# Kernel tuning notes

Measured on AMD Instinct MI355X. Metric: run time of the kernel, lower is better.

The kernel has to match this reference:

```python
import jax, jax.numpy as jnp
import numpy as np

EPS = 1e-6

def _conv1x1(x, w, b):
    # x: [b,c,h,w], w: [o,c], b: [o] -> per-pixel matmul
    return jnp.einsum('bchw,oc->bohw', x, w) + b[None, :, None, None]

def setup_inputs() -> dict:
    key = jax.random.key(0)
    ks = jax.random.split(key, 10)
    b, c, h, w = 16, 256, 128, 128
    dec = jax.random.normal(ks[0], (b, c, h, w), jnp.float32)
    enc = jax.random.normal(ks[1], (b, c, h, w), jnp.float32)
    ln_w = jnp.ones((c,), jnp.float32)
    ln_b = jnp.zeros((c,), jnp.float32)
    w0 = jax.random.normal(ks[2], (c, c), jnp.float32) * 0.05
    b0 = jax.random.normal(ks[3], (c,), jnp.float32) * 0.05
    w1 = jax.random.normal(ks[4], (c // 2, c), jnp.float32) * 0.05
    b1 = jax.random.normal(ks[5], (c // 2,), jnp.float32) * 0.05
    w2 = jax.random.normal(ks[6], (c // 4, c // 2), jnp.float32) * 0.05
    b2 = jax.random.normal(ks[7], (c // 4,), jnp.float32) * 0.05
    w3 = jax.random.normal(ks[8], (1, c // 4), jnp.float32) * 0.05
    b3 = jax.random.normal(ks[9], (1,), jnp.float32) * 0.05
    return dict(dec=dec, enc=enc, ln_w=ln_w, ln_b=ln_b, w0=w0, b0=b0,
                w1=w1, b1=b1, w2=w2, b2=b2, w3=w3, b3=b3)

def reference(dec, enc, ln_w, ln_b, w0, b0, w1, b1, w2, b2, w3, b3):
    b, c, h, w = dec.shape
    x = dec + enc
    # LayerNorm2d: normalize over channel dim per pixel (biased var, eps=1e-6)
    mu = jnp.mean(x, axis=1, keepdims=True)
    var = jnp.var(x, axis=1, keepdims=True)
    x = (x - mu) / jnp.sqrt(var + EPS) * ln_w[None, :, None, None] + ln_b[None, :, None, None]
    # in_conv: 1x1 conv + exact GELU
    x = jax.nn.gelu(_conv1x1(x, w0, b0), approximate=False)
    # split: local channels kept, global channels pooled and broadcast back
    local_x = x[:, :c // 2]                                   # [b,c/2,h,w]
    global_x = jnp.mean(x[:, c // 2:], axis=(2, 3), keepdims=True)  # [b,c/2,1,1]
    x = jnp.concatenate([local_x, jnp.broadcast_to(global_x, local_x.shape)], axis=1)
    # mask_pre: nc -> nc/2 -> nc/4 -> 1 with GELUs
    x = jax.nn.gelu(_conv1x1(x, w1, b1), approximate=False)
    x = jax.nn.gelu(_conv1x1(x, w2, b2), approximate=False)
    x = _conv1x1(x, w3, b3)
    return jax.nn.sigmoid(x)
```

## Files before the change

kernel.cpp:

```cpp
#include <hip/hip_runtime.h>
#include <math.h>

typedef float f32x4 __attribute__((ext_vector_type(4)));
typedef short s8v __attribute__((ext_vector_type(8)));

#define LN_EPS 1e-6f

static __device__ __forceinline__ unsigned short f2bf(float f) {
  union { float f; unsigned int u; } v; v.f = f;
  unsigned int r = (v.u + 0x7FFFu + ((v.u >> 16) & 1u)) >> 16;
  return (unsigned short)r;
}
static __device__ __forceinline__ float bf2f(unsigned short b) {
  union { float f; unsigned int u; } v; v.u = ((unsigned int)b) << 16;
  return v.f;
}
static __device__ __forceinline__ float gelu_exact(float x) {
  return 0.5f * x * (1.0f + erff(x * 0.70710678118654752f));
}

__global__ void prep_kernel(const float* __restrict__ w0, const float* __restrict__ w1,
                            const float* __restrict__ w2,
                            unsigned short* __restrict__ wt0f, unsigned short* __restrict__ w1f,
                            unsigned short* __restrict__ w2f, float* __restrict__ gacc) {
  int idx = blockIdx.x * blockDim.x + threadIdx.x;
  int stride = gridDim.x * blockDim.x;
  const int N0 = 65536, N1 = 16384, N2 = 8192, N3 = 2048;
  for (int i = idx; i < N0 + N1 + N2 + N3; i += stride) {
    if (i < N0) {
      int j = i & 7, l = (i >> 3) & 63, ks = (i >> 9) & 7, n0 = i >> 12;
      wt0f[i] = f2bf(w0[(n0 * 16 + (l & 15)) * 256 + ks * 32 + (l >> 4) * 8 + j]);
    } else if (i < N0 + N1) {
      int t = i - N0;
      int j = t & 7, l = (t >> 3) & 63, ks = (t >> 9) & 3, n0 = t >> 11;
      w1f[t] = f2bf(w1[(n0 * 16 + (l & 15)) * 256 + ks * 32 + (l >> 4) * 8 + j]);
    } else if (i < N0 + N1 + N2) {
      int t = i - N0 - N1;
      int j = t & 7, l = (t >> 3) & 63, ks = (t >> 9) & 3, n0 = t >> 11;
      w2f[t] = f2bf(w2[(n0 * 16 + (l & 15)) * 128 + ks * 32 + (l >> 4) * 8 + j]);
    } else {
      gacc[i - N0 - N1 - N2] = 0.0f;
    }
  }
}

__global__ __launch_bounds__(256, 2) void k1_kernel(
    const float* __restrict__ dec, const float* __restrict__ enc,
    const float* __restrict__ lnw, const float* __restrict__ lnb,
    const float* __restrict__ b0, const unsigned short* __restrict__ wt0f,
    unsigned short* __restrict__ yl, float* __restrict__ gacc) {
  __shared__ __align__(16) unsigned char At[64 * 512];
  __shared__ float red[16][16][8];
  __shared__ float muL[64], rsL[64];
  __shared__ float lnwS[256], lnbS[256];

  const int tid = threadIdx.x;
  const int blk = blockIdx.x;
  const int b = blk >> 8;
  const int hw0 = (blk & 255) << 6;
  const int g = tid >> 4, kq = tid & 15;
  const int lane = tid & 63, w = tid >> 6;
  const int l15 = lane & 15, lg = lane >> 4;

  lnwS[tid] = lnw[tid];
  lnbS[tid] = lnb[tid];

  f32x4 xv[16];
  f32x4 sum = {0.f, 0.f, 0.f, 0.f}, sq = {0.f, 0.f, 0.f, 0.f};
  const int baseoff = (b * 256) * 16384 + hw0 + (kq << 2);
#pragma unroll
  for (int it = 0; it < 2; ++it) {
#pragma unroll
    for (int s = 0; s < 8; ++s) {
      int c = it * 128 + g * 8 + s;
      f32x4 d = *(const f32x4*)(dec + baseoff + c * 16384);
      f32x4 e = *(const f32x4*)(enc + baseoff + c * 16384);
      f32x4 x = d + e;
      xv[it * 8 + s] = x;
      sum += x;
      sq += x * x;
    }
  }
#pragma unroll
  for (int q = 0; q < 4; ++q) { red[g][kq][q] = sum[q]; red[g][kq][4 + q] = sq[q]; }
  __syncthreads();
  if (tid < 64) {
    int p = tid, kk = p >> 2, comp = p & 3;
    float s = 0.f, s2 = 0.f;
#pragma unroll
    for (int gg = 0; gg < 16; ++gg) { s += red[gg][kk][comp]; s2 += red[gg][kk][4 + comp]; }
    float mu = s * (1.0f / 256.0f);
    float var = s2 * (1.0f / 256.0f) - mu * mu;
    muL[p] = mu;
    rsL[p] = rsqrtf(var + LN_EPS);
  }
  __syncthreads();

#pragma unroll
  for (int it = 0; it < 2; ++it) {
    int c0 = it * 128 + g * 8;
#pragma unroll
    for (int px = 0; px < 4; ++px) {
      int p = (kq << 2) + px;
      float mu = muL[p], rs = rsL[p];
      s8v hv;
#pragma unroll
      for (int s = 0; s < 8; ++s) {
        float x = xv[it * 8 + s][px];
        hv[s] = (short)f2bf((x - mu) * rs * lnwS[c0 + s] + lnbS[c0 + s]);
      }
      int byte = (p * 512 + c0 * 2) ^ ((p & 7) << 4);
      *(s8v*)(&At[byte]) = hv;
    }
  }
  __syncthreads();

  f32x4 acc[4][4];
#pragma unroll
  for (int mi = 0; mi < 4; ++mi)
#pragma unroll
    for (int ni = 0; ni < 4; ++ni) acc[mi][ni] = (f32x4){0.f, 0.f, 0.f, 0.f};

#pragma unroll
  for (int ks = 0; ks < 8; ++ks) {
    s8v a[4];
#pragma unroll
    for (int mi = 0; mi < 4; ++mi) {
      int p = mi * 16 + l15;
      int byte = (p * 512 + ks * 64 + lg * 16) ^ ((p & 7) << 4);
      a[mi] = *(const s8v*)(&At[byte]);
    }
#pragma unroll
    for (int ni = 0; ni < 4; ++ni) {
      int n0 = w * 4 + ni;
      s8v bfr = *(const s8v*)(wt0f + ((n0 * 8 + ks) * 64 + lane) * 8);
#pragma unroll
      for (int mi = 0; mi < 4; ++mi)
        acc[mi][ni] = __builtin_amdgcn_mfma_f32_16x16x32_bf16(a[mi], bfr, acc[mi][ni], 0, 0, 0);
    }
  }

  float bias[4];
#pragma unroll
  for (int ni = 0; ni < 4; ++ni) bias[ni] = b0[w * 64 + ni * 16 + l15];

  if (w < 2) {
#pragma unroll
    for (int mi = 0; mi < 4; ++mi) {
#pragma unroll
      for (int r = 0; r < 4; ++r) {
        int p = mi * 16 + lg * 4 + r;
        int prow = (b * 16384 + hw0 + p) * 128;
#pragma unroll
        for (int ni = 0; ni < 4; ++ni) {
          float v = gelu_exact(acc[mi][ni][r] + bias[ni]);
          yl[prow + w * 64 + ni * 16 + l15] = f2bf(v);
        }
      }
    }
  } else {
#pragma unroll
    for (int ni = 0; ni < 4; ++ni) {
      float ps = 0.f;
#pragma unroll
      for (int mi = 0; mi < 4; ++mi)
#pragma unroll
        for (int r = 0; r < 4; ++r)
          ps += gelu_exact(acc[mi][ni][r] + bias[ni]);
      ps += __shfl_xor(ps, 16, 64);
      ps += __shfl_xor(ps, 32, 64);
      if (lane < 16) atomicAdd(&gacc[b * 128 + (w - 2) * 64 + ni * 16 + lane], ps);
    }
  }
}

__global__ void kmid_kernel(const float* __restrict__ w1, const float* __restrict__ b1,
                            const float* __restrict__ gacc, float* __restrict__ g1) {
  int b = blockIdx.x, o = threadIdx.x;
  float acc = b1[o];
  const float inv = 1.0f / 16384.0f;
  for (int c = 0; c < 128; ++c)
    acc += w1[o * 256 + 128 + c] * (gacc[b * 128 + c] * inv);
  g1[b * 128 + o] = acc;
}

__global__ __launch_bounds__(256, 4) void k2_kernel(
    const unsigned short* __restrict__ yl, const float* __restrict__ g1,
    const float* __restrict__ b2v, const float* __restrict__ w3,
    const float* __restrict__ b3, const unsigned short* __restrict__ w1f,
    const unsigned short* __restrict__ w2f, float* __restrict__ out) {
  __shared__ __align__(16) unsigned char Yt[64 * 256];
  __shared__ __align__(16) unsigned char Z1[64 * 256];
  __shared__ __align__(16) unsigned char Z2[64 * 128];
  __shared__ float part3[4][64];
  __shared__ float w3S[64];

  const int tid = threadIdx.x, blk = blockIdx.x;
  const int lane = tid & 63, w = tid >> 6, l15 = lane & 15, lg = lane >> 4;
  const int P0 = blk * 64;
  const int b = blk >> 8;

  if (tid < 64) w3S[tid] = w3[tid];

#pragma unroll
  for (int q = 0; q < 4; ++q) {
    int p = q * 16 + (tid >> 4);
    int c2 = (tid & 15) * 16;
    s8v v = *(const s8v*)((const char*)yl + (long)(P0 + p) * 256 + c2);
    int byte = (p * 256 + c2) ^ ((p & 7) << 4);
    *(s8v*)(&Yt[byte]) = v;
  }
  __syncthreads();

  f32x4 acc1[4][2];
#pragma unroll
  for (int mi = 0; mi < 4; ++mi)
#pragma unroll
    for (int ni = 0; ni < 2; ++ni) acc1[mi][ni] = (f32x4){0.f, 0.f, 0.f, 0.f};
#pragma unroll
  for (int ks = 0; ks < 4; ++ks) {
    s8v a[4];
#pragma unroll
    for (int mi = 0; mi < 4; ++mi) {
      int p = mi * 16 + l15;
      int byte = (p * 256 + ks * 64 + lg * 16) ^ ((p & 7) << 4);
      a[mi] = *(const s8v*)(&Yt[byte]);
    }
#pragma unroll
    for (int ni = 0; ni < 2; ++ni) {
      int n0 = w * 2 + ni;
      s8v bfr = *(const s8v*)(w1f + ((n0 * 4 + ks) * 64 + lane) * 8);
#pragma unroll
      for (int mi = 0; mi < 4; ++mi)
        acc1[mi][ni] = __builtin_amdgcn_mfma_f32_16x16x32_bf16(a[mi], bfr, acc1[mi][ni], 0, 0, 0);
    }
  }
#pragma unroll
  for (int ni = 0; ni < 2; ++ni) {
    int o = (w * 2 + ni) * 16 + l15;
    float bias = g1[b * 128 + o];
#pragma unroll
    for (int mi = 0; mi < 4; ++mi)
#pragma unroll
      for (int r = 0; r < 4; ++r) {
        int p = mi * 16 + lg * 4 + r;
        float v = gelu_exact(acc1[mi][ni][r] + bias);
        int byte = (p * 256 + o * 2) ^ ((p & 7) << 4);
        *(unsigned short*)(&Z1[byte]) = f2bf(v);
      }
  }
  __syncthreads();

  f32x4 acc2[4];
#pragma unroll
  for (int mi = 0; mi < 4; ++mi) acc2[mi] = (f32x4){0.f, 0.f, 0.f, 0.f};
#pragma unroll
  for (int ks = 0; ks < 4; ++ks) {
    s8v a[4];
#pragma unroll
    for (int mi = 0; mi < 4; ++mi) {
      int p = mi * 16 + l15;
      int byte = (p * 256 + ks * 64 + lg * 16) ^ ((p & 7) << 4);
      a[mi] = *(const s8v*)(&Z1[byte]);
    }
    s8v bfr = *(const s8v*)(w2f + ((w * 4 + ks) * 64 + lane) * 8);
#pragma unroll
    for (int mi = 0; mi < 4; ++mi)
      acc2[mi] = __builtin_amdgcn_mfma_f32_16x16x32_bf16(a[mi], bfr, acc2[mi], 0, 0, 0);
  }
  {
    int o = w * 16 + l15;
    float bias = b2v[o];
#pragma unroll
    for (int mi = 0; mi < 4; ++mi)
#pragma unroll
      for (int r = 0; r < 4; ++r) {
        int p = mi * 16 + lg * 4 + r;
        float v = gelu_exact(acc2[mi][r] + bias);
        int byte = (p * 128 + o * 2) ^ ((p & 7) << 4);
        *(unsigned short*)(&Z2[byte]) = f2bf(v);
      }
  }
  __syncthreads();

  {
    int p = tid & 63, cg = tid >> 6;
    float dot = 0.f;
#pragma unroll
    for (int half = 0; half < 2; ++half) {
      int byte = (p * 128 + cg * 32 + half * 16) ^ ((p & 7) << 4);
      s8v z = *(const s8v*)(&Z2[byte]);
#pragma unroll
      for (int j = 0; j < 8; ++j)
        dot += bf2f((unsigned short)z[j]) * w3S[cg * 16 + half * 8 + j];
    }
    part3[cg][p] = dot;
  }
  __syncthreads();
  if (tid < 64) {
    float t = part3[0][tid] + part3[1][tid] + part3[2][tid] + part3[3][tid] + b3[0];
    out[P0 + tid] = 1.0f / (1.0f + expf(-t));
  }
}

extern "C" void kernel_launch(void* const* d_in, const int* in_sizes, int n_in,
                              void* d_out, int out_size, void* d_ws, size_t ws_size,
                              hipStream_t stream) {
  const float* dec = (const float*)d_in[0];
  const float* enc = (const float*)d_in[1];
  const float* lnw = (const float*)d_in[2];
  const float* lnb = (const float*)d_in[3];
  const float* w0  = (const float*)d_in[4];
  const float* b0  = (const float*)d_in[5];
  const float* w1  = (const float*)d_in[6];
  const float* b1  = (const float*)d_in[7];
  const float* w2  = (const float*)d_in[8];
  const float* b2  = (const float*)d_in[9];
  const float* w3  = (const float*)d_in[10];
  const float* b3  = (const float*)d_in[11];

  char* ws = (char*)d_ws;
  unsigned short* yl   = (unsigned short*)ws;
  unsigned short* wt0f = (unsigned short*)(ws + 67108864);
  unsigned short* w1f  = (unsigned short*)(ws + 67239936);
  unsigned short* w2f  = (unsigned short*)(ws + 67272704);
  float* gacc          = (float*)(ws + 67289088);
  float* g1            = (float*)(ws + 67297280);

  prep_kernel<<<128, 256, 0, stream>>>(w0, w1, w2, wt0f, w1f, w2f, gacc);
  k1_kernel<<<4096, 256, 0, stream>>>(dec, enc, lnw, lnb, b0, wt0f, yl, gacc);
  kmid_kernel<<<16, 128, 0, stream>>>(w1, b1, gacc, g1);
  k2_kernel<<<4096, 256, 0, stream>>>(yl, g1, b2, w3, b3, w1f, w2f, (float*)d_out);
}
```

Measured before the change: 229.4 us.

## Fold LayerNorm affine into conv weights and halve k1 pixel tile

Folds the LayerNorm scale into the first conv weights in the prep kernel, plus per-output sums for the shift and bias. The GEMM therefore runs on raw (dec+enc) cast to bf16, and normalization is applied afterwards as acc*rs + (-mu*rs)*s + t. k1 now handles 32 pixels per block instead of 64, uses wave shuffles instead of a large LDS reduction, removes a barrier before the LDS store, and raises the occupancy target to 6 blocks. The risk is precision: quantizing unnormalized x to bf16 and subtracting the mean after the GEMM can cancel badly when the mean is large relative to the spread. Halving the tile also doubles weight-fragment reloads per pixel.

```diff
diff --git a/kernel.cpp b/kernel.cpp
--- a/kernel.cpp
+++ b/kernel.cpp
@@ -20,16 +20,19 @@
 }
 
 __global__ void prep_kernel(const float* __restrict__ w0, const float* __restrict__ w1,
-                            const float* __restrict__ w2,
+                            const float* __restrict__ w2, const float* __restrict__ lnw,
+                            const float* __restrict__ lnb, const float* __restrict__ b0,
                             unsigned short* __restrict__ wt0f, unsigned short* __restrict__ w1f,
-                            unsigned short* __restrict__ w2f, float* __restrict__ gacc) {
+                            unsigned short* __restrict__ w2f, float* __restrict__ gacc,
+                            float* __restrict__ sfold, float* __restrict__ tfold) {
   int idx = blockIdx.x * blockDim.x + threadIdx.x;
   int stride = gridDim.x * blockDim.x;
-  const int N0 = 65536, N1 = 16384, N2 = 8192, N3 = 2048;
-  for (int i = idx; i < N0 + N1 + N2 + N3; i += stride) {
+  const int N0 = 65536, N1 = 16384, N2 = 8192, N3 = 2048, N4 = 256;
+  for (int i = idx; i < N0 + N1 + N2 + N3 + N4; i += stride) {
     if (i < N0) {
       int j = i & 7, l = (i >> 3) & 63, ks = (i >> 9) & 7, n0 = i >> 12;
-      wt0f[i] = f2bf(w0[(n0 * 16 + (l & 15)) * 256 + ks * 32 + (l >> 4) * 8 + j]);
+      int k = ks * 32 + (l >> 4) * 8 + j;
+      wt0f[i] = f2bf(w0[(n0 * 16 + (l & 15)) * 256 + k] * lnw[k]);
     } else if (i < N0 + N1) {
       int t = i - N0;
       int j = t & 7, l = (t >> 3) & 63, ks = (t >> 9) & 3, n0 = t >> 11;
@@ -38,138 +41,158 @@
       int t = i - N0 - N1;
       int j = t & 7, l = (t >> 3) & 63, ks = (t >> 9) & 3, n0 = t >> 11;
       w2f[t] = f2bf(w2[(n0 * 16 + (l & 15)) * 128 + ks * 32 + (l >> 4) * 8 + j]);
+    } else if (i < N0 + N1 + N2 + N3) {
+      gacc[i - N0 - N1 - N2] = 0.0f;
     } else {
-      gacc[i - N0 - N1 - N2] = 0.0f;
-    }
-  }
-}
-
-__global__ __launch_bounds__(256, 2) void k1_kernel(
+      int n = i - N0 - N1 - N2 - N3;
+      float s = 0.f, t = 0.f;
+      for (int c = 0; c < 256; ++c) {
+        float wv = w0[n * 256 + c];
+        s += wv * lnw[c];
+        t += wv * lnb[c];
+      }
+      sfold[n] = s;
+      tfold[n] = t + b0[n];
+    }
+  }
+}
+
+__global__ __launch_bounds__(256, 6) void k1_kernel(
     const float* __restrict__ dec, const float* __restrict__ enc,
-    const float* __restrict__ lnw, const float* __restrict__ lnb,
-    const float* __restrict__ b0, const unsigned short* __restrict__ wt0f,
+    const unsigned short* __restrict__ wt0f,
+    const float* __restrict__ sfold, const float* __restrict__ tfold,
     unsigned short* __restrict__ yl, float* __restrict__ gacc) {
-  __shared__ __align__(16) unsigned char At[64 * 512];
-  __shared__ float red[16][16][8];
-  __shared__ float muL[64], rsL[64];
-  __shared__ float lnwS[256], lnbS[256];
-
-  const int tid = threadIdx.x;
-  const int blk = blockIdx.x;
-  const int b = blk >> 8;
-  const int hw0 = (blk & 255) << 6;
-  const int g = tid >> 4, kq = tid & 15;
-  const int lane = tid & 63, w = tid >> 6;
-  const int l15 = lane & 15, lg = lane >> 4;
-
-  lnwS[tid] = lnw[tid];
-  lnbS[tid] = lnb[tid];
-
-  f32x4 xv[16];
+  __shared__ __align__(16) unsigned char At[32 * 512];
+  __shared__ float wred[4][8][8];
+  __shared__ float alphaL[32], betaL[32];
+
+  const int tid = threadIdx.x, blk = blockIdx.x;
+  const int b = blk >> 9;
+  const int hw0 = (blk & 511) << 5;
+  const int g = tid >> 3, kq = tid & 7;
+  const int lane = tid & 63, w = tid >> 6, l15 = lane & 15, lg = lane >> 4;
+
+  f32x4 xv[8];
   f32x4 sum = {0.f, 0.f, 0.f, 0.f}, sq = {0.f, 0.f, 0.f, 0.f};
-  const int baseoff = (b * 256) * 16384 + hw0 + (kq << 2);
-#pragma unroll
-  for (int it = 0; it < 2; ++it) {
-#pragma unroll
-    for (int s = 0; s < 8; ++s) {
-      int c = it * 128 + g * 8 + s;
-      f32x4 d = *(const f32x4*)(dec + baseoff + c * 16384);
-      f32x4 e = *(const f32x4*)(enc + baseoff + c * 16384);
-      f32x4 x = d + e;
-      xv[it * 8 + s] = x;
-      sum += x;
-      sq += x * x;
-    }
-  }
-#pragma unroll
-  for (int q = 0; q < 4; ++q) { red[g][kq][q] = sum[q]; red[g][kq][4 + q] = sq[q]; }
-  __syncthreads();
-  if (tid < 64) {
-    int p = tid, kk = p >> 2, comp = p & 3;
+  const long base = (long)(b * 256) * 16384 + hw0 + (kq << 2);
+#pragma unroll
+  for (int s = 0; s < 8; ++s) {
+    const int c = g * 8 + s;
+    f32x4 d = *(const f32x4*)(dec + base + (long)c * 16384);
+    f32x4 e = *(const f32x4*)(enc + base + (long)c * 16384);
+    f32x4 x = d + e;
+    xv[s] = x;
+    sum += x;
+    sq += x * x;
+  }
+#pragma unroll
+  for (int px = 0; px < 4; ++px) {
+    const int p = (kq << 2) + px;
+    s8v hv;
+#pragma unroll
+    for (int s = 0; s < 8; ++s) hv[s] = (short)f2bf(xv[s][px]);
+    const int byte = (p * 512 + g * 16) ^ ((p & 7) << 4);
+    *(s8v*)(&At[byte]) = hv;
+  }
+
+#pragma unroll
+  for (int dd = 8; dd <= 32; dd <<= 1) {
+#pragma unroll
+    for (int q = 0; q < 4; ++q) {
+      sum[q] += __shfl_xor(sum[q], dd, 64);
+      sq[q] += __shfl_xor(sq[q], dd, 64);
+    }
+  }
+  if (lane < 8) {
+#pragma unroll
+    for (int q = 0; q < 4; ++q) { wred[w][lane][q] = sum[q]; wred[w][lane][4 + q] = sq[q]; }
+  }
+  __syncthreads();
+  if (tid < 32) {
+    const int kk = tid >> 2, q = tid & 3;
     float s = 0.f, s2 = 0.f;
 #pragma unroll
-    for (int gg = 0; gg < 16; ++gg) { s += red[gg][kk][comp]; s2 += red[gg][kk][4 + comp]; }
-    float mu = s * (1.0f / 256.0f);
-    float var = s2 * (1.0f / 256.0f) - mu * mu;
-    muL[p] = mu;
-    rsL[p] = rsqrtf(var + LN_EPS);
-  }
-  __syncthreads();
-
-#pragma unroll
-  for (int it = 0; it < 2; ++it) {
-    int c0 = it * 128 + g * 8;
-#pragma unroll
-    for (int px = 0; px < 4; ++px) {
-      int p = (kq << 2) + px;
-      float mu = muL[p], rs = rsL[p];
-      s8v hv;
-#pragma unroll
-      for (int s = 0; s < 8; ++s) {
-        float x = xv[it * 8 + s][px];
-        hv[s] = (short)f2bf((x - mu) * rs * lnwS[c0 + s] + lnbS[c0 + s]);
-      }
-      int byte = (p * 512 + c0 * 2) ^ ((p & 7) << 4);
-      *(s8v*)(&At[byte]) = hv;
-    }
-  }
-  __syncthreads();
-
-  f32x4 acc[4][4];
-#pragma unroll
-  for (int mi = 0; mi < 4; ++mi)
+    for (int ww = 0; ww < 4; ++ww) { s += wred[ww][kk][q]; s2 += wred[ww][kk][4 + q]; }
+    const float mu = s * (1.0f / 256.0f);
+    const float var = s2 * (1.0f / 256.0f) - mu * mu;
+    const float rs = rsqrtf(var + LN_EPS);
+    alphaL[tid] = rs;
+    betaL[tid] = -mu * rs;
+  }
+  __syncthreads();
+
+  f32x4 acc[2][4];
+#pragma unroll
+  for (int mi = 0; mi < 2; ++mi)
 #pragma unroll
     for (int ni = 0; ni < 4; ++ni) acc[mi][ni] = (f32x4){0.f, 0.f, 0.f, 0.f};
 
 #pragma unroll
   for (int ks = 0; ks < 8; ++ks) {
-    s8v a[4];
-#pragma unroll
-    for (int mi = 0; mi < 4; ++mi) {
-      int p = mi * 16 + l15;
-      int byte = (p * 512 + ks * 64 + lg * 16) ^ ((p & 7) << 4);
+    s8v a[2];
+#pragma unroll
+    for (int mi = 0; mi < 2; ++mi) {
+      const int p = mi * 16 + l15;
+      const int byte = (p * 512 + ks * 64 + lg * 16) ^ ((p & 7) << 4);
       a[mi] = *(const s8v*)(&At[byte]);
     }
 #pragma unroll
     for (int ni = 0; ni < 4; ++ni) {
-      int n0 = w * 4 + ni;
+      const int n0 = w * 4 + ni;
       s8v bfr = *(const s8v*)(wt0f + ((n0 * 8 + ks) * 64 + lane) * 8);
 #pragma unroll
-      for (int mi = 0; mi < 4; ++mi)
+      for (int mi = 0; mi < 2; ++mi)
         acc[mi][ni] = __builtin_amdgcn_mfma_f32_16x16x32_bf16(a[mi], bfr, acc[mi][ni], 0, 0, 0);
     }
   }
 
-  float bias[4];
-#pragma unroll
-  for (int ni = 0; ni < 4; ++ni) bias[ni] = b0[w * 64 + ni * 16 + l15];
+  float sn[4], tn[4];
+#pragma unroll
+  for (int ni = 0; ni < 4; ++ni) {
+    const int n = w * 64 + ni * 16 + l15;
+    sn[ni] = sfold[n];
+    tn[ni] = tfold[n];
+  }
+  const f32x4 al0 = *(const f32x4*)(&alphaL[lg * 4]);
+  const f32x4 al1 = *(const f32x4*)(&alphaL[16 + lg * 4]);
+  const f32x4 be0 = *(const f32x4*)(&betaL[lg * 4]);
+  const f32x4 be1 = *(const f32x4*)(&betaL[16 + lg * 4]);
 
   if (w < 2) {
 #pragma unroll
-    for (int mi = 0; mi < 4; ++mi) {
+    for (int mi = 0; mi < 2; ++mi) {
 #pragma unroll
       for (int r = 0; r < 4; ++r) {
-        int p = mi * 16 + lg * 4 + r;
-        int prow = (b * 16384 + hw0 + p) * 128;
+        const int p = mi * 16 + lg * 4 + r;
+        const float al = mi ? al1[r] : al0[r];
+        const float be = mi ? be1[r] : be0[r];
+        const long prow = ((long)b * 16384 + hw0 + p) * 128;
 #pragma unroll
         for (int ni = 0; ni < 4; ++ni) {
-          float v = gelu_exact(acc[mi][ni][r] + bias[ni]);
+          const float v = gelu_exact(fmaf(al, acc[mi][ni][r], fmaf(be, sn[ni], tn[ni])));
           yl[prow + w * 64 + ni * 16 + l15] = f2bf(v);
         }
       }
     }
   } else {
+    float ps[4] = {0.f, 0.f, 0.f, 0.f};
+#pragma unroll
+    for (int mi = 0; mi < 2; ++mi) {
+#pragma unroll
+      for (int r = 0; r < 4; ++r) {
+        const float al = mi ? al1[r] : al0[r];
+        const float be = mi ? be1[r] : be0[r];
+#pragma unroll
+        for (int ni = 0; ni < 4; ++ni)
+          ps[ni] += gelu_exact(fmaf(al, acc[mi][ni][r], fmaf(be, sn[ni], tn[ni])));
+      }
+    }
 #pragma unroll
     for (int ni = 0; ni < 4; ++ni) {
-      float ps = 0.f;
-#pragma unroll
-      for (int mi = 0; mi < 4; ++mi)
-#pragma unroll
-        for (int r = 0; r < 4; ++r)
-          ps += gelu_exact(acc[mi][ni][r] + bias[ni]);
-      ps += __shfl_xor(ps, 16, 64);
-      ps += __shfl_xor(ps, 32, 64);
-      if (lane < 16) atomicAdd(&gacc[b * 128 + (w - 2) * 64 + ni * 16 + lane], ps);
+      float p2 = ps[ni];
+      p2 += __shfl_xor(p2, 16, 64);
+      p2 += __shfl_xor(p2, 32, 64);
+      if (lane < 16) atomicAdd(&gacc[b * 128 + (w - 2) * 64 + ni * 16 + lane], p2);
     }
   }
 }
@@ -326,9 +349,12 @@
   unsigned short* w2f  = (unsigned short*)(ws + 67272704);
   float* gacc          = (float*)(ws + 67289088);
   float* g1            = (float*)(ws + 67297280);
-
-  prep_kernel<<<128, 256, 0, stream>>>(w0, w1, w2, wt0f, w1f, w2f, gacc);
-  k1_kernel<<<4096, 256, 0, stream>>>(dec, enc, lnw, lnb, b0, wt0f, yl, gacc);
+  float* sfold         = (float*)(ws + 67305472);
+  float* tfold         = (float*)(ws + 67306496);
+
+  prep_kernel<<<128, 256, 0, stream>>>(w0, w1, w2, lnw, lnb, b0, wt0f, w1f, w2f,
+                                       gacc, sfold, tfold);
+  k1_kernel<<<8192, 256, 0, stream>>>(dec, enc, wt0f, sfold, tfold, yl, gacc);
   kmid_kernel<<<16, 128, 0, stream>>>(w1, b1, gacc, g1);
   k2_kernel<<<4096, 256, 0, stream>>>(yl, g1, b2, w3, b3, w1f, w2f, (float*)d_out);
 }
```

New measurement: 311.5 us. 1.36x slower.
